# Kernel optimization log

Measured on AMD Instinct MI355X. Metric: run time of the kernel, lower is better.

Reference implementation:

```python
import jax, jax.numpy as jnp
import numpy as np

MUL = 512
DIMS = (1, 3, 5, 7)  # dims of irreps 0e,1o,2e,3o
N = 8192
TOTAL = MUL * sum(DIMS)  # 8192


def setup_inputs() -> dict:
    key = jax.random.key(0)
    ks = jax.random.split(key, 5)
    inp = {"x": jax.random.normal(ks[0], (N, TOTAL), dtype=jnp.float32)}
    for i in range(4):
        inp[f"w{i}"] = jax.random.normal(ks[i + 1], (MUL, MUL), dtype=jnp.float32)
    return inp


def reference(x, w0, w1, w2, w3):
    # Block-diagonal equivariant linear: for each irrep segment (mul_ir layout),
    # mix multiplicities with a (mul_in, mul_out) weight shared across the
    # (2l+1) irrep components, scaled by 1/sqrt(mul_in).
    ws = (w0, w1, w2, w3)
    scale = 1.0 / np.sqrt(MUL)
    outs = []
    off = 0
    for d, w in zip(DIMS, ws):
        seg = x[:, off:off + MUL * d].reshape(N, MUL, d)  # [N, mul, d]
        o = jnp.einsum('nud,uv->nvd', seg, w,
                       precision=jax.lax.Precision.HIGH) * scale
        outs.append(o.reshape(N, MUL * d))
        off += MUL * d
    return jnp.concatenate(outs, axis=1)  # [N, TOTAL]
```

## Files before the change

kernel.cpp:

```cpp
#include <hip/hip_runtime.h>
#include <hip/hip_bf16.h>
#include <stdint.h>

typedef float  f32x4   __attribute__((ext_vector_type(4)));
typedef short  short8  __attribute__((ext_vector_type(8)));
typedef short  short4v __attribute__((ext_vector_type(4)));

#define TOTAL 8192

__device__ __forceinline__ void dma16(const void* g, void* l) {
  __builtin_amdgcn_global_load_lds(
      (const __attribute__((address_space(1))) unsigned int*)g,
      (__attribute__((address_space(3))) unsigned int*)l,
      16, 0, 0);
}

__global__ __launch_bounds__(256) void prep_wt(
    const float* __restrict__ w0, const float* __restrict__ w1,
    const float* __restrict__ w2, const float* __restrict__ w3,
    __hip_bfloat16* __restrict__ wt) {
  __shared__ float T[64][65];
  const int s = blockIdx.z;
  const float* w = (s == 0) ? w0 : (s == 1) ? w1 : (s == 2) ? w2 : w3;
  const int u0 = blockIdx.y * 64, v0 = blockIdx.x * 64;
  const int tx = threadIdx.x & 63, ty = threadIdx.x >> 6;
#pragma unroll
  for (int k = 0; k < 16; ++k) {
    int r = ty * 16 + k;
    T[r][tx] = w[(size_t)(u0 + r) * 512 + v0 + tx];
  }
  __syncthreads();
  const float scale = 0.04419417382415922f;
#pragma unroll
  for (int k = 0; k < 16; ++k) {
    int r = ty * 16 + k;
    wt[((size_t)s << 18) + (size_t)(v0 + r) * 512 + u0 + tx] =
        __float2bfloat16(T[tx][r] * scale);
  }
}

template <int D, int SEGOFF>
__device__ __forceinline__ void seg_gemm(
    const float* __restrict__ x, const __hip_bfloat16* __restrict__ wt,
    float* __restrict__ out, int rt) {
  constexpr int BM = 64, BK = 32, LDA = BK + 8;
  constexpr int CHUNK = BK * D;
  extern __shared__ char smem[];
  __hip_bfloat16* As = (__hip_bfloat16*)smem;
  __hip_bfloat16* Bs = (__hip_bfloat16*)(smem + BM * LDA * 2);

  const int tid  = threadIdx.x;
  const int lane = tid & 63;
  const int wv   = tid >> 6;
  const int row0 = rt * BM;
  const int nF   = row0 / D;
  const int nL   = (row0 + BM - 1) / D;
  const int F4   = ((nL - nF + 1) * CHUNK) >> 2;
  const int q  = lane >> 4, cl = lane & 15;

  f32x4 acc[4][8] = {};

  for (int k0 = 0; k0 < 512; k0 += BK) {
    __syncthreads();
    for (int e = tid; e < F4; e += 256) {
      int p4 = e << 2;
      int nb = p4 / CHUNK;
      int p  = p4 - nb * CHUNK;
      int n  = nF + nb;
      const float* gp = x + (size_t)n * TOTAL + SEGOFF + k0 * D + p;
      float4 vv = *(const float4*)gp;
      if (D == 1) {
        int r = n - row0;
        if ((unsigned)r < (unsigned)BM) {
          __hip_bfloat16 tmp[4];
          tmp[0] = __float2bfloat16(vv.x); tmp[1] = __float2bfloat16(vv.y);
          tmp[2] = __float2bfloat16(vv.z); tmp[3] = __float2bfloat16(vv.w);
          *(short4v*)&As[r * LDA + p] = *(const short4v*)tmp;
        }
      } else {
        const float* vf = (const float*)&vv;
#pragma unroll
        for (int c = 0; c < 4; ++c) {
          int pc = p + c;
          int u  = pc / D;
          int j  = pc - u * D;
          int r  = n * D + j - row0;
          if ((unsigned)r < (unsigned)BM)
            As[r * LDA + u] = __float2bfloat16(vf[c]);
        }
      }
    }
#pragma unroll
    for (int t = 0; t < 8; ++t) {
      int i    = wv * 8 + t;
      int vrow = i * 16 + (lane >> 2);
      const __hip_bfloat16* gs = wt + (size_t)vrow * 512 + k0 + ((lane & 3) << 3);
      dma16(gs, Bs + i * 512);
    }
    __syncthreads();
    short8 afr[4];
#pragma unroll
    for (int mi = 0; mi < 4; ++mi) {
      const __hip_bfloat16* pa = As + (mi * 16 + cl) * LDA + q * 8;
      short4v lo = *(const short4v*)pa;
      short4v hi = *(const short4v*)(pa + 4);
      afr[mi] = __builtin_shufflevector(lo, hi, 0, 1, 2, 3, 4, 5, 6, 7);
    }
#pragma unroll
    for (int ni = 0; ni < 8; ++ni) {
      const __hip_bfloat16* pb = Bs + (size_t)(wv * 128 + ni * 16 + cl) * BK + q * 8;
      short8 bfr = *(const short8*)pb;
#pragma unroll
      for (int mi = 0; mi < 4; ++mi)
        acc[mi][ni] = __builtin_amdgcn_mfma_f32_16x16x32_bf16(afr[mi], bfr, acc[mi][ni], 0, 0, 0);
    }
  }
#pragma unroll
  for (int mi = 0; mi < 4; ++mi) {
#pragma unroll
    for (int ni = 0; ni < 8; ++ni) {
#pragma unroll
      for (int rg = 0; rg < 4; ++rg) {
        int R = row0 + mi * 16 + q * 4 + rg;
        int n = R / D;
        int j = R - n * D;
        int v = wv * 128 + ni * 16 + cl;
        out[(size_t)n * TOTAL + SEGOFF + v * D + j] = acc[mi][ni][rg];
      }
    }
  }
}

__global__ __launch_bounds__(256, 2) void linear_main(
    const float* __restrict__ x, const __hip_bfloat16* __restrict__ wt,
    float* __restrict__ out) {
  int bx = blockIdx.x;
  if (bx < 128)        seg_gemm<1, 0>   (x, wt,             out, bx);
  else if (bx < 512)   seg_gemm<3, 512> (x, wt + (1 << 18), out, bx - 128);
  else if (bx < 1152)  seg_gemm<5, 2048>(x, wt + (2 << 18), out, bx - 512);
  else                 seg_gemm<7, 4608>(x, wt + (3 << 18), out, bx - 1152);
}

extern "C" void kernel_launch(void* const* d_in, const int* in_sizes, int n_in,
                              void* d_out, int out_size, void* d_ws, size_t ws_size,
                              hipStream_t stream) {
  const float* x  = (const float*)d_in[0];
  const float* w0 = (const float*)d_in[1];
  const float* w1 = (const float*)d_in[2];
  const float* w2 = (const float*)d_in[3];
  const float* w3 = (const float*)d_in[4];
  __hip_bfloat16* wt = (__hip_bfloat16*)d_ws;
  float* out = (float*)d_out;

  hipLaunchKernelGGL(prep_wt, dim3(8, 8, 4), dim3(256), 0, stream,
                     w0, w1, w2, w3, wt);
  hipLaunchKernelGGL(linear_main, dim3(2048), dim3(256), 37888, stream,
                     x, wt, out);
}
```

Measured before the change: 615.4 us.

## Double-buffer A/B tiles in LDS and XOR-swizzle the weight layout

```diff
diff --git a/kernel.cpp b/kernel.cpp
--- a/kernel.cpp
+++ b/kernel.cpp
@@ -31,10 +31,13 @@
   }
   __syncthreads();
   const float scale = 0.04419417382415922f;
+  const int ksw_base = (tx & ~31) | (tx & 7);
+  const int kch = (tx >> 3) & 3;
 #pragma unroll
   for (int k = 0; k < 16; ++k) {
     int r = ty * 16 + k;
-    wt[((size_t)s << 18) + (size_t)(v0 + r) * 512 + u0 + tx] =
+    int ksw = ksw_base | ((kch ^ ((r >> 1) & 3)) << 3);
+    wt[((size_t)s << 18) + (size_t)(v0 + r) * 512 + u0 + ksw] =
         __float2bfloat16(T[tx][r] * scale);
   }
 }
@@ -45,9 +48,12 @@
     float* __restrict__ out, int rt) {
   constexpr int BM = 64, BK = 32, LDA = BK + 8;
   constexpr int CHUNK = BK * D;
+  constexpr int ASZ = BM * LDA;
+  constexpr int BSZ = 512 * BK;
+  constexpr int NPF = (D == 1) ? 2 : 3;
   extern __shared__ char smem[];
   __hip_bfloat16* As = (__hip_bfloat16*)smem;
-  __hip_bfloat16* Bs = (__hip_bfloat16*)(smem + BM * LDA * 2);
+  __hip_bfloat16* Bs = (__hip_bfloat16*)(smem + 2 * ASZ * 2);
 
   const int tid  = threadIdx.x;
   const int lane = tid & 63;
@@ -57,64 +63,95 @@
   const int nL   = (row0 + BM - 1) / D;
   const int F4   = ((nL - nF + 1) * CHUNK) >> 2;
   const int q  = lane >> 4, cl = lane & 15;
+  const int slotx = (q ^ ((cl >> 1) & 3)) << 3;
 
   f32x4 acc[4][8] = {};
 
-  for (int k0 = 0; k0 < 512; k0 += BK) {
-    __syncthreads();
-    for (int e = tid; e < F4; e += 256) {
-      int p4 = e << 2;
-      int nb = p4 / CHUNK;
-      int p  = p4 - nb * CHUNK;
-      int n  = nF + nb;
-      const float* gp = x + (size_t)n * TOTAL + SEGOFF + k0 * D + p;
-      float4 vv = *(const float4*)gp;
-      if (D == 1) {
-        int r = n - row0;
-        if ((unsigned)r < (unsigned)BM) {
-          __hip_bfloat16 tmp[4];
-          tmp[0] = __float2bfloat16(vv.x); tmp[1] = __float2bfloat16(vv.y);
-          tmp[2] = __float2bfloat16(vv.z); tmp[3] = __float2bfloat16(vv.w);
-          *(short4v*)&As[r * LDA + p] = *(const short4v*)tmp;
-        }
-      } else {
-        const float* vf = (const float*)&vv;
-#pragma unroll
-        for (int c = 0; c < 4; ++c) {
-          int pc = p + c;
-          int u  = pc / D;
-          int j  = pc - u * D;
-          int r  = n * D + j - row0;
-          if ((unsigned)r < (unsigned)BM)
-            As[r * LDA + u] = __float2bfloat16(vf[c]);
-        }
+  auto loadA = [&](int e, int k0) -> float4 {
+    int p4 = e << 2;
+    int nb = p4 / CHUNK;
+    int p  = p4 - nb * CHUNK;
+    int n  = nF + nb;
+    return *(const float4*)(x + (size_t)n * TOTAL + SEGOFF + k0 * D + p);
+  };
+  auto storeA = [&](__hip_bfloat16* Ab, int e, float4 vv) {
+    if (e >= F4) return;
+    int p4 = e << 2;
+    int nb = p4 / CHUNK;
+    int p  = p4 - nb * CHUNK;
+    int n  = nF + nb;
+    if (D == 1) {
+      int r = n - row0;
+      if ((unsigned)r < (unsigned)BM) {
+        __hip_bfloat16 tmp[4];
+        tmp[0] = __float2bfloat16(vv.x); tmp[1] = __float2bfloat16(vv.y);
+        tmp[2] = __float2bfloat16(vv.z); tmp[3] = __float2bfloat16(vv.w);
+        *(short4v*)&Ab[r * LDA + p] = *(const short4v*)tmp;
       }
-    }
-#pragma unroll
-    for (int t = 0; t < 8; ++t) {
-      int i    = wv * 8 + t;
+    } else {
+      const float* vf = (const float*)&vv;
+#pragma unroll
+      for (int c = 0; c < 4; ++c) {
+        int pc = p + c;
+        int u  = pc / D;
+        int j  = pc - u * D;
+        int r  = n * D + j - row0;
+        if ((unsigned)r < (unsigned)BM)
+          Ab[r * LDA + u] = __float2bfloat16(vf[c]);
+      }
+    }
+  };
+  auto dmaB = [&](__hip_bfloat16* Bb, int k0) {
+#pragma unroll
+    for (int t8 = 0; t8 < 8; ++t8) {
+      int i = wv * 8 + t8;
       int vrow = i * 16 + (lane >> 2);
-      const __hip_bfloat16* gs = wt + (size_t)vrow * 512 + k0 + ((lane & 3) << 3);
-      dma16(gs, Bs + i * 512);
-    }
-    __syncthreads();
+      dma16(wt + (size_t)vrow * 512 + k0 + ((lane & 3) << 3), Bb + i * 512);
+    }
+  };
+
+  for (int e = tid; e < F4; e += 256) storeA(As, e, loadA(e, 0));
+  dmaB(Bs, 0);
+  __syncthreads();
+
+#pragma unroll 2
+  for (int t = 0; t < 16; ++t) {
+    const int cur = t & 1;
+    const int k0n = ((t + 1) & 15) * BK;
+    __hip_bfloat16* Ac = As + cur * ASZ;
+    __hip_bfloat16* Bc = Bs + cur * BSZ;
+    __hip_bfloat16* An = As + (cur ^ 1) * ASZ;
+    __hip_bfloat16* Bn = Bs + (cur ^ 1) * BSZ;
+
+    float4 pf[NPF];
+#pragma unroll
+    for (int i = 0; i < NPF; ++i) {
+      int e = tid + (i << 8);
+      pf[i] = loadA(e < F4 ? e : 0, k0n);
+    }
+    dmaB(Bn, k0n);
+
     short8 afr[4];
 #pragma unroll
     for (int mi = 0; mi < 4; ++mi) {
-      const __hip_bfloat16* pa = As + (mi * 16 + cl) * LDA + q * 8;
+      const __hip_bfloat16* pa = Ac + (mi * 16 + cl) * LDA + q * 8;
       short4v lo = *(const short4v*)pa;
       short4v hi = *(const short4v*)(pa + 4);
       afr[mi] = __builtin_shufflevector(lo, hi, 0, 1, 2, 3, 4, 5, 6, 7);
     }
 #pragma unroll
     for (int ni = 0; ni < 8; ++ni) {
-      const __hip_bfloat16* pb = Bs + (size_t)(wv * 128 + ni * 16 + cl) * BK + q * 8;
-      short8 bfr = *(const short8*)pb;
+      const short8 bfr = *(const short8*)(Bc + (wv * 128 + ni * 16 + cl) * BK + slotx);
 #pragma unroll
       for (int mi = 0; mi < 4; ++mi)
         acc[mi][ni] = __builtin_amdgcn_mfma_f32_16x16x32_bf16(afr[mi], bfr, acc[mi][ni], 0, 0, 0);
     }
-  }
+
+#pragma unroll
+    for (int i = 0; i < NPF; ++i) storeA(An, tid + (i << 8), pf[i]);
+    __syncthreads();
+  }
+
 #pragma unroll
   for (int mi = 0; mi < 4; ++mi) {
 #pragma unroll
@@ -140,6 +177,8 @@
   else if (bx < 1152)  seg_gemm<5, 2048>(x, wt + (2 << 18), out, bx - 512);
   else                 seg_gemm<7, 4608>(x, wt + (3 << 18), out, bx - 1152);
 }
+
+#define LDS_BYTES 75776
 
 extern "C" void kernel_launch(void* const* d_in, const int* in_sizes, int n_in,
                               void* d_out, int out_size, void* d_ws, size_t ws_size,
@@ -152,8 +191,11 @@
   __hip_bfloat16* wt = (__hip_bfloat16*)d_ws;
   float* out = (float*)d_out;
 
+  hipFuncSetAttribute((const void*)linear_main,
+                      hipFuncAttributeMaxDynamicSharedMemorySize, LDS_BYTES);
+
   hipLaunchKernelGGL(prep_wt, dim3(8, 8, 4), dim3(256), 0, stream,
                      w0, w1, w2, w3, wt);
-  hipLaunchKernelGGL(linear_main, dim3(2048), dim3(256), 37888, stream,
+  hipLaunchKernelGGL(linear_main, dim3(2048), dim3(256), LDS_BYTES, stream,
                      x, wt, out);
 }
```

Measured after the change: 543.1 us. 1.13x faster.
